# Kernel tuning notes

Measured on AMD Instinct MI355X. Metric: run time of the kernel, lower is better.

The kernel has to match this reference:

```python
import jax, jax.numpy as jnp
import numpy as np

B, L, C = 4, 6400, 768
HS, WS = 80, 80
NH, NP, NL = 6, 4, 1
DH = C // NH
EPS = 1e-6


def setup_inputs() -> dict:
    key = jax.random.key(0)
    ks = jax.random.split(key, 10)
    p = lambda k, shape: jax.random.normal(k, shape, jnp.float32) * 0.02
    return {
        "x": jax.random.normal(ks[0], (B, L, C), jnp.float32),
        "reference_points": jax.random.uniform(ks[1], (B, L, NL, 2), dtype=jnp.float32),
        "feat": jax.random.normal(ks[2], (B, L, C), jnp.float32),
        "spatial_shapes": jnp.array([[HS, WS]], jnp.int32),
        "level_start_index": jnp.array([0], jnp.int32),
        "qn_w": jnp.ones((C,), jnp.float32), "qn_b": jnp.zeros((C,), jnp.float32),
        "fn_w": jnp.ones((C,), jnp.float32), "fn_b": jnp.zeros((C,), jnp.float32),
        "gamma": p(ks[3], (C,)),
        "Wv": p(ks[4], (C, C)), "bv": jnp.zeros((C,), jnp.float32),
        "Woff": p(ks[5], (C, NH * NL * NP * 2)), "boff": p(ks[6], (NH * NL * NP * 2,)),
        "Waw": p(ks[7], (C, NH * NL * NP)), "baw": jnp.zeros((NH * NL * NP,), jnp.float32),
        "Wout": p(ks[8], (C, C)), "bout": jnp.zeros((C,), jnp.float32),
    }


def layernorm(x, w, b):
    mu = jnp.mean(x, -1, keepdims=True)
    var = jnp.mean((x - mu) ** 2, -1, keepdims=True)
    return (x - mu) * jax.lax.rsqrt(var + EPS) * w + b


def ms_deform_attn(q, reference_points, f, spatial_shapes, level_start_index,
                   Wv, bv, Woff, boff, Waw, baw, Wout, bout):
    shapes = np.asarray(spatial_shapes)      # static metadata (concrete)
    starts = np.asarray(level_start_index)
    value = (f @ Wv + bv).reshape(B, L, NH, DH)
    offs = (q @ Woff + boff).reshape(B, L, NH, NL, NP, 2)
    aw = jax.nn.softmax((q @ Waw + baw).reshape(B, L, NH, NL * NP), axis=-1)
    aw = aw.reshape(B, L, NH, NL, NP)
    # offset normalizer is (W, H) per level
    normalizer = jnp.stack([spatial_shapes[:, 1], spatial_shapes[:, 0]], -1).astype(q.dtype)
    loc = reference_points[:, :, None, :, None, :] + offs / normalizer[None, None, None, :, None, :]

    gat = jax.vmap(jax.vmap(lambda vv, ii: vv[ii]))  # over batch, then head
    levels = []
    for l in range(shapes.shape[0]):
        H_, W_ = int(shapes[l, 0]), int(shapes[l, 1])
        s0 = int(starts[l])
        v = value[:, s0:s0 + H_ * W_].transpose(0, 2, 1, 3)  # [B,NH,HW,DH]
        # grid_sample align_corners=False pixel coords
        lx = loc[:, :, :, l, :, 0] * W_ - 0.5                # [B,L,NH,NP]
        ly = loc[:, :, :, l, :, 1] * H_ - 0.5
        x0 = jnp.floor(lx); y0 = jnp.floor(ly)
        tx, ty = lx - x0, ly - y0
        x0i, y0i = x0.astype(jnp.int32), y0.astype(jnp.int32)
        acc = jnp.zeros((B, NH, L, NP, DH), value.dtype)
        for dy, wy in ((0, 1.0 - ty), (1, ty)):
            for dx, wx in ((0, 1.0 - tx), (1, tx)):
                xi, yi = x0i + dx, y0i + dy
                valid = (xi >= 0) & (xi < W_) & (yi >= 0) & (yi < H_)  # zero padding
                idx = (jnp.clip(yi, 0, H_ - 1) * W_ + jnp.clip(xi, 0, W_ - 1)).transpose(0, 2, 1, 3)
                w = (wx * wy * valid).transpose(0, 2, 1, 3)           # [B,NH,L,NP]
                acc = acc + gat(v, idx) * w[..., None]
        levels.append(acc)                                            # [B,NH,L,NP,DH]
    samp = jnp.stack(levels, axis=3)                                  # [B,NH,L,NL,NP,DH]
    out = jnp.einsum('bhqlpd,bqhlp->bqhd', samp, aw).reshape(B, L, C)
    return out @ Wout + bout


def reference(x, reference_points, feat, spatial_shapes, level_start_index,
              qn_w, qn_b, fn_w, fn_b, gamma, Wv, bv, Woff, boff, Waw, baw, Wout, bout):
    q = layernorm(x, qn_w, qn_b)
    f = layernorm(feat, fn_w, fn_b)
    attn = ms_deform_attn(q, reference_points, f, spatial_shapes, level_start_index,
                          Wv, bv, Woff, boff, Waw, baw, Wout, bout)
    return x + gamma * attn
```

## Files before the change

kernel.cpp:

```cpp
#include <hip/hip_runtime.h>
#include <hip/hip_bf16.h>

#define B_  4
#define L_  6400
#define C_  768
#define NH_ 6
#define NP_ 4
#define DH_ 128
#define HW_ 80
#define M_  (B_*L_)

using f32x4  = float __attribute__((ext_vector_type(4)));
using bf16x8 = short __attribute__((ext_vector_type(8)));

#define AS1(p) ((const __attribute__((address_space(1))) void*)(p))
#define AS3(p) ((__attribute__((address_space(3))) void*)(p))

__device__ __forceinline__ ushort f2bf(float f) {
    __hip_bfloat16 h = __float2bfloat16(f);
    return *reinterpret_cast<ushort*>(&h);
}
__device__ __forceinline__ float bf2f(ushort u) {
    union { unsigned u; float f; } v; v.u = ((unsigned)u) << 16; return v.f;
}

__global__ __launch_bounds__(256) void prep_weights(
    const float* __restrict__ Wv, const float* __restrict__ Woff,
    const float* __restrict__ Waw, const float* __restrict__ boff,
    const float* __restrict__ baw, const float* __restrict__ Wout,
    ushort* __restrict__ Wv_t, ushort* __restrict__ Wout_t,
    ushort* __restrict__ Wcomb_t, float* __restrict__ comb_bias)
{
    int i = blockIdx.x * 256 + threadIdx.x;
    const int WSZ = C_ * C_;
    if (i < WSZ) {
        int n = i / C_, k = i % C_;
        Wv_t[i]   = f2bf(Wv[k * C_ + n]);
        Wout_t[i] = f2bf(Wout[k * C_ + n]);
    } else {
        int j = i - WSZ;
        if (j < 128 * C_) {
            int n = j / C_, k = j % C_;
            float v = 0.f;
            if (n < 48)      v = Woff[k * 48 + n];
            else if (n < 72) v = Waw[k * 24 + (n - 48)];
            Wcomb_t[j] = f2bf(v);
        }
    }
    if (i < 128) {
        float v = 0.f;
        if (i < 48)      v = boff[i];
        else if (i < 72) v = baw[i - 48];
        comb_bias[i] = v;
    }
}

__global__ __launch_bounds__(256) void ln_kernel(
    const float* __restrict__ x, const float* __restrict__ feat,
    const float* __restrict__ qw, const float* __restrict__ qb,
    const float* __restrict__ fw, const float* __restrict__ fb,
    ushort* __restrict__ q, ushort* __restrict__ fn)
{
    int wave = threadIdx.x >> 6, lane = threadIdx.x & 63;
    long r = (long)blockIdx.x * 4 + wave;
    const float* in; ushort* out; const float* w; const float* b;
    if (r < M_) { in = x + r * C_;          out = q  + r * C_;          w = qw; b = qb; }
    else        { long rr = r - M_; in = feat + rr * C_; out = fn + rr * C_; w = fw; b = fb; }

    const float4* in4 = (const float4*)in;
    float4 v[3];
    float s = 0.f, s2 = 0.f;
#pragma unroll
    for (int i = 0; i < 3; i++) {
        v[i] = in4[lane + 64 * i];
        s  += v[i].x + v[i].y + v[i].z + v[i].w;
        s2 += v[i].x*v[i].x + v[i].y*v[i].y + v[i].z*v[i].z + v[i].w*v[i].w;
    }
#pragma unroll
    for (int off = 32; off; off >>= 1) { s += __shfl_xor(s, off); s2 += __shfl_xor(s2, off); }
    float mean = s * (1.f / C_);
    float var  = s2 * (1.f / C_) - mean * mean;
    float rs   = rsqrtf(var + 1e-6f);
#pragma unroll
    for (int i = 0; i < 3; i++) {
        int c = (lane + 64 * i) * 4;
        ushort4 o;
        o.x = f2bf((v[i].x - mean) * rs * w[c + 0] + b[c + 0]);
        o.y = f2bf((v[i].y - mean) * rs * w[c + 1] + b[c + 1]);
        o.z = f2bf((v[i].z - mean) * rs * w[c + 2] + b[c + 2]);
        o.w = f2bf((v[i].w - mean) * rs * w[c + 3] + b[c + 3]);
        ((ushort4*)out)[lane + 64 * i] = o;
    }
}

template<int MODE>
__global__ __launch_bounds__(256) void gemm_bf16(
    const ushort* __restrict__ A, const ushort* __restrict__ Bt,
    const float* __restrict__ bias, void* __restrict__ Cout,
    const float* __restrict__ xres, const float* __restrict__ gamma,
    int ldc)
{
    const int K = C_;
    __shared__ ushort As[128][32];
    __shared__ ushort Bs[128][32];
    const int m0 = blockIdx.y * 128;
    const int n0 = blockIdx.x * 128;
    const int t   = threadIdx.x;
    const int w   = t >> 6, lane = t & 63;
    const int WR = (w >> 1) * 64, WC = (w & 1) * 64;
    const int rowA0 = t >> 2;
    const int colA  = (t & 3) * 8;
    const int row15 = lane & 15, kb = (lane >> 4) * 8;

    f32x4 acc[4][4] = {};
    char* ldsA = (char*)As;
    char* ldsB = (char*)Bs;

    for (int k0 = 0; k0 < K; k0 += 32) {
        __syncthreads();
#pragma unroll
        for (int c = 0; c < 2; c++) {
            const ushort* ga = A  + (long)(m0 + c * 64 + rowA0) * K + k0 + colA;
            const ushort* gb = Bt + (long)(n0 + c * 64 + rowA0) * K + k0 + colA;
            __builtin_amdgcn_global_load_lds(AS1(ga), AS3(ldsA + c * 4096 + w * 1024), 16, 0, 0);
            __builtin_amdgcn_global_load_lds(AS1(gb), AS3(ldsB + c * 4096 + w * 1024), 16, 0, 0);
        }
        __syncthreads();
        bf16x8 af[4], bfr[4];
#pragma unroll
        for (int m = 0; m < 4; m++) af[m]  = *(bf16x8*)&As[WR + m * 16 + row15][kb];
#pragma unroll
        for (int n = 0; n < 4; n++) bfr[n] = *(bf16x8*)&Bs[WC + n * 16 + row15][kb];
#pragma unroll
        for (int m = 0; m < 4; m++)
#pragma unroll
            for (int n = 0; n < 4; n++)
                acc[m][n] = __builtin_amdgcn_mfma_f32_16x16x32_bf16(af[m], bfr[n], acc[m][n], 0, 0, 0);
    }

    const int rbase = (lane >> 4) * 4;
    const int cbase = lane & 15;
    const int bblk = m0 / L_;
#pragma unroll
    for (int m = 0; m < 4; m++)
#pragma unroll
    for (int n = 0; n < 4; n++) {
        int gcol = n0 + WC + n * 16 + cbase;
        float bb = bias[gcol];
#pragma unroll
        for (int j = 0; j < 4; j++) {
            int grow = m0 + WR + m * 16 + rbase + j;
            float vv = acc[m][n][j] + bb;
            if (MODE == 0) {
                int l = grow - bblk * L_;
                int h = gcol >> 7, d = gcol & 127;
                long o = (((long)bblk * NH_ + h) * L_ + l) * DH_ + d;
                ((ushort*)Cout)[o] = f2bf(vv);
            } else if (MODE == 1) {
                ((float*)Cout)[(long)grow * ldc + gcol] = vv;
            } else {
                long o = (long)grow * C_ + gcol;
                ((float*)Cout)[o] = xres[o] + gamma[gcol] * vv;
            }
        }
    }
}

__global__ __launch_bounds__(256) void loc_kernel(
    const float* __restrict__ scores,
    const float* __restrict__ refp,
    float4* __restrict__ samp)
{
    int wave = threadIdx.x >> 6, lane = threadIdx.x & 63;
    long row = (long)blockIdx.x * 4 + wave;
    if (lane >= 24) return;
    const float* sc = scores + row * 128;
    int h = lane >> 2, p = lane & 3;
    float ox = sc[h * 8 + p * 2], oy = sc[h * 8 + p * 2 + 1];
    float logit = sc[48 + lane];
    float m = logit;
    m = fmaxf(m, __shfl_xor(m, 1));
    m = fmaxf(m, __shfl_xor(m, 2));
    float e = expf(logit - m);
    float ssum = e;
    ssum += __shfl_xor(ssum, 1);
    ssum += __shfl_xor(ssum, 2);
    float w = e / ssum;
    float rx = refp[row * 2], ry = refp[row * 2 + 1];
    samp[row * 24 + lane] = make_float4(rx * HW_ + ox - 0.5f, ry * HW_ + oy - 0.5f, w, 0.f);
}

__global__ __launch_bounds__(256) void sample_kernel(
    const ushort* __restrict__ value_t,
    const float4* __restrict__ samp,
    ushort* __restrict__ attn_out)
{
    int bid = (int)(blockIdx.x & 7) * 1200 + (int)(blockIdx.x >> 3);
    int t = threadIdx.x;
    int grp = t >> 4;
    int d16 = t & 15;
    int gid = bid * 16 + grp;
    int bh = gid / L_;  int l = gid - bh * L_;
    int b  = bh / NH_;  int h = bh - b * NH_;
    const ushort* plane = value_t + (long)bh * (HW_ * HW_) * DH_ + d16 * 8;
    long bl = (long)b * L_ + l;
    const float4* sp = samp + bl * 24 + h * 4;

    float acc[8] = {};
#pragma unroll
    for (int p = 0; p < 4; p++) {
        float4 s = sp[p];
        float lx = s.x, ly = s.y, wgt = s.z;
        float x0f = floorf(lx), y0f = floorf(ly);
        float tx = lx - x0f, ty = ly - y0f;
        int x0 = (int)x0f, y0 = (int)y0f;
#pragma unroll
        for (int dy = 0; dy < 2; dy++) {
            int yi = y0 + dy;
            float wy = dy ? ty : 1.f - ty;
#pragma unroll
            for (int dx = 0; dx < 2; dx++) {
                int xi = x0 + dx;
                float wx = dx ? tx : 1.f - tx;
                bool valid = (xi >= 0) & (xi < HW_) & (yi >= 0) & (yi < HW_);
                float wc = valid ? (wgt * wy * wx) : 0.f;
                int yc = min(max(yi, 0), HW_ - 1);
                int xc = min(max(xi, 0), HW_ - 1);
                uint4 v = *(const uint4*)(plane + (long)(yc * HW_ + xc) * DH_);
                const unsigned* u = (const unsigned*)&v;
#pragma unroll
                for (int i = 0; i < 4; i++) {
                    union { unsigned q; float f; } lo, hi;
                    lo.q = u[i] << 16;
                    hi.q = u[i] & 0xffff0000u;
                    acc[2 * i]     += wc * lo.f;
                    acc[2 * i + 1] += wc * hi.f;
                }
            }
        }
    }
    bf16x8 o;
#pragma unroll
    for (int i = 0; i < 8; i++) o[i] = (short)f2bf(acc[i]);
    *(bf16x8*)(attn_out + bl * C_ + h * DH_ + d16 * 8) = o;
}

extern "C" void kernel_launch(void* const* d_in, const int* in_sizes, int n_in,
                              void* d_out, int out_size, void* d_ws, size_t ws_size,
                              hipStream_t stream) {
    const float* x     = (const float*)d_in[0];
    const float* refp  = (const float*)d_in[1];
    const float* feat  = (const float*)d_in[2];
    const float* qn_w  = (const float*)d_in[5];
    const float* qn_b  = (const float*)d_in[6];
    const float* fn_w  = (const float*)d_in[7];
    const float* fn_b  = (const float*)d_in[8];
    const float* gamma = (const float*)d_in[9];
    const float* Wv    = (const float*)d_in[10];
    const float* bv    = (const float*)d_in[11];
    const float* Woff  = (const float*)d_in[12];
    const float* boff  = (const float*)d_in[13];
    const float* Waw   = (const float*)d_in[14];
    const float* baw   = (const float*)d_in[15];
    const float* Wout  = (const float*)d_in[16];
    const float* bout  = (const float*)d_in[17];

    char* ws = (char*)d_ws;
    size_t off = 0;
    auto alloc = [&](size_t bytes) -> void* {
        void* p = ws + off; off += (bytes + 255) & ~(size_t)255; return p;
    };
    ushort* q       = (ushort*)alloc((size_t)M_ * C_ * 2);
    ushort* fn      = (ushort*)alloc((size_t)M_ * C_ * 2);
    ushort* value_t = (ushort*)alloc((size_t)M_ * C_ * 2);
    float4* samp    = (float4*)alloc((size_t)M_ * 24 * 16);
    ushort* Wv_t    = (ushort*)alloc((size_t)C_ * C_ * 2);
    ushort* Wout_t  = (ushort*)alloc((size_t)C_ * C_ * 2);
    ushort* Wcomb_t = (ushort*)alloc((size_t)128 * C_ * 2);
    float*  cbias   = (float*)alloc(128 * 4);
    float*  scores   = (float*)fn;
    ushort* attn_out = q;

    prep_weights<<<2688, 256, 0, stream>>>(Wv, Woff, Waw, boff, baw, Wout,
                                           Wv_t, Wout_t, Wcomb_t, cbias);
    ln_kernel<<<(2 * M_) / 4, 256, 0, stream>>>(x, feat, qn_w, qn_b, fn_w, fn_b, q, fn);
    gemm_bf16<0><<<dim3(6, 200), 256, 0, stream>>>(fn, Wv_t, bv, value_t, nullptr, nullptr, C_);
    gemm_bf16<1><<<dim3(1, 200), 256, 0, stream>>>(q, Wcomb_t, cbias, scores, nullptr, nullptr, 128);
    loc_kernel<<<M_ / 4, 256, 0, stream>>>(scores, refp, samp);
    sample_kernel<<<(M_ * NH_) / 16, 256, 0, stream>>>(value_t, samp, attn_out);
    gemm_bf16<2><<<dim3(6, 200), 256, 0, stream>>>(attn_out, Wout_t, bout, d_out, x, gamma, C_);
}
```

Baseline: 433.4 us.

## Double-buffer GEMM LDS tiles and swizzle block order across XCDs

```diff
diff --git a/kernel.cpp b/kernel.cpp
--- a/kernel.cpp
+++ b/kernel.cpp
@@ -98,13 +98,18 @@
     const ushort* __restrict__ A, const ushort* __restrict__ Bt,
     const float* __restrict__ bias, void* __restrict__ Cout,
     const float* __restrict__ xres, const float* __restrict__ gamma,
-    int ldc)
-{
-    const int K = C_;
-    __shared__ ushort As[128][32];
-    __shared__ ushort Bs[128][32];
-    const int m0 = blockIdx.y * 128;
-    const int n0 = blockIdx.x * 128;
+    int ldc, int nbx)
+{
+    const int K = C_, BK = 32, NT = K / BK;
+    __shared__ ushort As[2][128][32];
+    __shared__ ushort Bs[2][128][32];
+    const int nwg = gridDim.x;
+    const int per = nwg >> 3;
+    const int bid = (int)blockIdx.x;
+    const int swz = (bid & 7) * per + (bid >> 3);
+    const int by = swz / nbx, bx = swz - by * nbx;
+    const int m0 = by * 128;
+    const int n0 = bx * 128;
     const int t   = threadIdx.x;
     const int w   = t >> 6, lane = t & 63;
     const int WR = (w >> 1) * 64, WC = (w & 1) * 64;
@@ -113,29 +118,38 @@
     const int row15 = lane & 15, kb = (lane >> 4) * 8;
 
     f32x4 acc[4][4] = {};
-    char* ldsA = (char*)As;
-    char* ldsB = (char*)Bs;
-
-    for (int k0 = 0; k0 < K; k0 += 32) {
-        __syncthreads();
+
+    auto STAGE = [&](int buf, int k0) {
 #pragma unroll
         for (int c = 0; c < 2; c++) {
             const ushort* ga = A  + (long)(m0 + c * 64 + rowA0) * K + k0 + colA;
             const ushort* gb = Bt + (long)(n0 + c * 64 + rowA0) * K + k0 + colA;
-            __builtin_amdgcn_global_load_lds(AS1(ga), AS3(ldsA + c * 4096 + w * 1024), 16, 0, 0);
-            __builtin_amdgcn_global_load_lds(AS1(gb), AS3(ldsB + c * 4096 + w * 1024), 16, 0, 0);
+            __builtin_amdgcn_global_load_lds(AS1(ga), AS3((char*)As + buf * 8192 + c * 4096 + w * 1024), 16, 0, 0);
+            __builtin_amdgcn_global_load_lds(AS1(gb), AS3((char*)Bs + buf * 8192 + c * 4096 + w * 1024), 16, 0, 0);
         }
-        __syncthreads();
+    };
+    auto COMPUTE = [&](int buf) {
         bf16x8 af[4], bfr[4];
 #pragma unroll
-        for (int m = 0; m < 4; m++) af[m]  = *(bf16x8*)&As[WR + m * 16 + row15][kb];
-#pragma unroll
-        for (int n = 0; n < 4; n++) bfr[n] = *(bf16x8*)&Bs[WC + n * 16 + row15][kb];
+        for (int m = 0; m < 4; m++) af[m]  = *(bf16x8*)&As[buf][WR + m * 16 + row15][kb];
+#pragma unroll
+        for (int n = 0; n < 4; n++) bfr[n] = *(bf16x8*)&Bs[buf][WC + n * 16 + row15][kb];
 #pragma unroll
         for (int m = 0; m < 4; m++)
 #pragma unroll
             for (int n = 0; n < 4; n++)
                 acc[m][n] = __builtin_amdgcn_mfma_f32_16x16x32_bf16(af[m], bfr[n], acc[m][n], 0, 0, 0);
+    };
+
+    STAGE(0, 0);
+    __syncthreads();
+    for (int kt = 0; kt < NT; kt += 2) {
+        STAGE(1, (kt + 1) * BK);
+        COMPUTE(0);
+        __syncthreads();
+        if (kt + 2 < NT) STAGE(0, (kt + 2) * BK);
+        COMPUTE(1);
+        __syncthreads();
     }
 
     const int rbase = (lane >> 4) * 4;
@@ -284,9 +298,9 @@
     prep_weights<<<2688, 256, 0, stream>>>(Wv, Woff, Waw, boff, baw, Wout,
                                            Wv_t, Wout_t, Wcomb_t, cbias);
     ln_kernel<<<(2 * M_) / 4, 256, 0, stream>>>(x, feat, qn_w, qn_b, fn_w, fn_b, q, fn);
-    gemm_bf16<0><<<dim3(6, 200), 256, 0, stream>>>(fn, Wv_t, bv, value_t, nullptr, nullptr, C_);
-    gemm_bf16<1><<<dim3(1, 200), 256, 0, stream>>>(q, Wcomb_t, cbias, scores, nullptr, nullptr, 128);
+    gemm_bf16<0><<<1200, 256, 0, stream>>>(fn, Wv_t, bv, value_t, nullptr, nullptr, C_, 6);
+    gemm_bf16<1><<<200, 256, 0, stream>>>(q, Wcomb_t, cbias, scores, nullptr, nullptr, 128, 1);
     loc_kernel<<<M_ / 4, 256, 0, stream>>>(scores, refp, samp);
     sample_kernel<<<(M_ * NH_) / 16, 256, 0, stream>>>(value_t, samp, attn_out);
-    gemm_bf16<2><<<dim3(6, 200), 256, 0, stream>>>(attn_out, Wout_t, bout, d_out, x, gamma, C_);
-}
+    gemm_bf16<2><<<1200, 256, 0, stream>>>(attn_out, Wout_t, bout, d_out, x, gamma, C_, 6);
+}
```

Measured after the change: 427.8 us. Within noise of the previous version (-1.3%).
